# Kernel optimization log

Measured on AMD Instinct MI355X. Metric: run time of the kernel, lower is better.

## Reference

```python
import jax, jax.numpy as jnp
import numpy as np

EPS = 1e-12
N, C, B = 8, 2048, 2048


def setup_inputs() -> dict:
    key = jax.random.key(0)
    kx, kk, kq = jax.random.split(key, 3)
    # Xavier-uniform bound for [C,C] weight
    bound = float(np.sqrt(6.0 / (C + C)))
    X = jax.random.normal(kx, (N, C, B), dtype=jnp.float32)
    Wk = jax.random.uniform(kk, (C, C), minval=-bound, maxval=bound, dtype=jnp.float32)
    Wq = jax.random.uniform(kq, (C, C), minval=-bound, maxval=bound, dtype=jnp.float32)
    Wk0 = jnp.zeros((C, 1), dtype=jnp.float32)
    Wq0 = jnp.zeros((C, 1), dtype=jnp.float32)
    return {"X": X, "Wk": Wk, "Wq": Wq, "Wk0": Wk0, "Wq0": Wq0}


def reference(X, Wk, Wq, Wk0, Wq0):
    # X: [N,C,B]; Wk,Wq: [C,C]; Wk0,Wq0: [C,1] (broadcast over B)
    K = jnp.einsum('ij,njb->nib', Wk, X) + Wk0  # [N,C,B]
    Q = jnp.einsum('ij,njb->nib', Wq, X) + Wq0  # [N,C,B]
    DK2 = jnp.sum(K * K, axis=2)  # [N,C] squared row norms
    DQ2 = jnp.sum(Q * Q, axis=2)  # [N,C]
    DQK = jnp.sqrt(jnp.maximum(DQ2[:, :, None] * DK2[:, None, :], EPS))  # [N,C,C]
    Y = jnp.einsum('nib,njb->nij', Q, K) / DQK  # cosine-normalized scores [N,C,C]
    SM = jax.nn.softmax(Y, axis=1)  # softmax over query-channel axis
    # Z = (X^T @ SM)^T : Z[n,j,b] = sum_c X[n,c,b] * SM[n,c,j]
    Z = jnp.einsum('ncb,ncj->njb', X, SM)  # [N,C,B]
    return Z
```

## Files before the change

kernel.cpp:

```cpp
#include <hip/hip_runtime.h>
#include <hip/hip_bf16.h>

typedef __bf16 bf16_t;
typedef __bf16 bf16x8 __attribute__((ext_vector_type(8)));
typedef __bf16 bf16x4 __attribute__((ext_vector_type(4)));
typedef float  f32x4  __attribute__((ext_vector_type(4)));

#define NB 8
#define CD 2048
#define BD 2048
#define LD 2048
#define BK 64
#define NT (LD / BK)
#define NP (NT / 2)

#define BAR()     __builtin_amdgcn_s_barrier()
#define WAITV(n)  asm volatile("s_waitcnt vmcnt(" #n ")" ::: "memory")
#define M_DSRD 0x100
#define M_MFMA 0x008

template <int NRD>
__device__ __forceinline__ void ilv_pattern() {
#pragma unroll
    for (int g = 0; g < 4; ++g) {
        __builtin_amdgcn_sched_group_barrier(M_DSRD, NRD, 0);
        __builtin_amdgcn_sched_group_barrier(M_MFMA, 4, 0);
    }
}

__global__ void k_transpose_x(const float* __restrict__ X, bf16_t* __restrict__ XbT) {
    __shared__ bf16_t tile[64][66];
    const int t = threadIdx.x;
    const int b0 = blockIdx.x * 64, c0 = blockIdx.y * 64, n = blockIdx.z;
    const float* Xn = X + (size_t)n * CD * BD;
    bf16_t* Tn = XbT + (size_t)n * BD * CD;
    const int cl = t & 63, rw = t >> 6;
#pragma unroll
    for (int r = 0; r < 16; ++r) {
        int row = r * 4 + rw;
        tile[row][cl] = (bf16_t)Xn[(size_t)(c0 + row) * BD + b0 + cl];
    }
    __syncthreads();
#pragma unroll
    for (int r = 0; r < 16; ++r) {
        int row = r * 4 + rw;
        Tn[(size_t)(b0 + row) * CD + c0 + cl] = tile[cl][row];
    }
}

__global__ void k_convert_w(const float* __restrict__ Wk, const float* __restrict__ Wq,
                            bf16_t* __restrict__ Wkb, bf16_t* __restrict__ Wqb) {
    const size_t i = ((size_t)blockIdx.x * 256 + threadIdx.x) * 4;
    const float* src = blockIdx.y ? Wq : Wk;
    bf16_t* dst = blockIdx.y ? Wqb : Wkb;
    float4 v = *(const float4*)(src + i);
    bf16x4 o;
    o[0] = (bf16_t)v.x; o[1] = (bf16_t)v.y; o[2] = (bf16_t)v.z; o[3] = (bf16_t)v.w;
    *(bf16x4*)(dst + i) = o;
}


__device__ __forceinline__ void gll16(const bf16_t* g, bf16_t* l) {
    __builtin_amdgcn_global_load_lds((const __attribute__((address_space(1))) void*)g,
                                     (__attribute__((address_space(3))) void*)l, 16, 0, 0);
}

__device__ __forceinline__ void stage_half(const bf16_t* gsrc, bf16_t* ldsh, int w, int l) {
    const int rr = l >> 3;
    const int ce = ((l & 7) ^ rr) * 8;
#pragma unroll
    for (int i = 0; i < 2; ++i) {
        const bf16_t* g = gsrc + (size_t)(i * 64 + w * 8 + rr) * LD + ce;
        gll16(g, ldsh + i * 4096 + w * 512);
    }
}

__device__ __forceinline__ bf16x8 lds_frag(const bf16_t* hbase, int row16, int lr, int st, int ks, int swz) {
    const int r = row16 + lr;
    const int ce = (st * 32 + ks * 8) ^ swz;
    return *(const bf16x8*)(hbase + r * 64 + ce);
}

template <int EPI>
__global__ __launch_bounds__(512, 2) void k_gemm256(const bf16_t* __restrict__ Aall, size_t sA,
                                                    const bf16_t* __restrict__ Ball, size_t sB,
                                                    void* __restrict__ Call, size_t sC,
                                                    const float* __restrict__ bias) {
    __shared__ alignas(16) bf16_t As[2][2][128 * 64];
    __shared__ alignas(16) bf16_t Bs[2][2][128 * 64];
    const int tid = threadIdx.x;
    const int lane = tid & 63, wave = tid >> 6;
    const int wm = wave >> 2, wn = wave & 3;
    const int lr = lane & 15, ks = lane >> 4;
    const int swz = (lr & 7) << 3;

    const int bid = blockIdx.x;
    const int lin = (bid & 7) * 64 + (bid >> 3);
    const int z = lin >> 6, rem = lin & 63, bm = rem >> 3, bn = rem & 7;
    const int m0 = bm * 256, n0 = bn * 256;

    const bf16_t* Ab = Aall + sA * z + (size_t)m0 * LD;
    const bf16_t* Bb = Ball + sB * z + (size_t)n0 * LD;

    stage_half(Ab,                 &As[0][0][0], wave, lane);
    stage_half(Bb,                 &Bs[0][0][0], wave, lane);
    stage_half(Ab + 128 * LD,      &As[0][1][0], wave, lane);
    stage_half(Bb + 128 * LD,      &Bs[0][1][0], wave, lane);
    WAITV(4);
    stage_half(Ab + BK,            &As[1][0][0], wave, lane);
    stage_half(Bb + BK,            &Bs[1][0][0], wave, lane);
    stage_half(Bb + 128 * LD + BK, &Bs[1][1][0], wave, lane);
    WAITV(6);
    BAR();

    f32x4 acc[2][2][4][2] = {};
    bf16x8 afrE[4][2], afrO[4][2], bf0[2][2], bf1[2][2];

    auto RD_A = [&](bf16x8 (&dst)[4][2], int slot, int half) {
#pragma unroll
        for (int mi = 0; mi < 4; ++mi)
#pragma unroll
            for (int st = 0; st < 2; ++st)
                dst[mi][st] = lds_frag(&As[slot][half][0], wm * 64 + mi * 16, lr, st, ks, swz);
    };
    auto RD_B = [&](bf16x8 (&dst)[2][2], int slot, int half) {
#pragma unroll
        for (int ni = 0; ni < 2; ++ni)
#pragma unroll
            for (int st = 0; st < 2; ++st)
                dst[ni][st] = lds_frag(&Bs[slot][half][0], wn * 32 + ni * 16, lr, st, ks, swz);
    };
    auto MFMA_Q = [&](int mh, int nh, bf16x8 (&asrc)[4][2], bf16x8 (&bsrc)[2][2]) {
#pragma unroll
        for (int st = 0; st < 2; ++st)
#pragma unroll
            for (int mi = 0; mi < 4; ++mi)
#pragma unroll
                for (int ni = 0; ni < 2; ++ni)
                    acc[mh][nh][mi][ni] = __builtin_amdgcn_mfma_f32_16x16x32_bf16(
                        asrc[mi][st], bsrc[ni][st], acc[mh][nh][mi][ni], 0, 0, 0);
    };

    RD_A(afrE, 0, 0); RD_B(bf0, 0, 0);

    for (int tp = 0; tp < NP; ++tp) {
        const int u = 2 * tp, v = u + 1;
        const int w = (u + 2 < NT) ? u + 2 : NT - 1;
        const int x = (v + 2 < NT) ? v + 2 : NT - 1;

        stage_half(Ab + 128 * LD + v * BK, &As[1][1][0], wave, lane);
        BAR();
        __builtin_amdgcn_s_setprio(1);
        RD_B(bf1, 0, 1);
        MFMA_Q(0, 0, afrE, bf0);
        ilv_pattern<1>();
        __builtin_amdgcn_s_setprio(0);
        BAR();

        stage_half(Ab + w * BK, &As[0][0][0], wave, lane);
        BAR();
        __builtin_amdgcn_s_setprio(1);
        RD_A(afrO, 0, 1);
        MFMA_Q(0, 1, afrE, bf1);
        ilv_pattern<2>();
        __builtin_amdgcn_s_setprio(0);
        BAR();

        stage_half(Bb + w * BK, &Bs[0][0][0], wave, lane);
        BAR();
        __builtin_amdgcn_s_setprio(1);
        MFMA_Q(1, 0, afrO, bf0);
        __builtin_amdgcn_s_setprio(0);
        BAR();

        stage_half(Bb + 128 * LD + w * BK, &Bs[0][1][0], wave, lane);
        WAITV(6);
        BAR();
        __builtin_amdgcn_s_setprio(1);
        RD_A(afrE, 1, 0); RD_B(bf0, 1, 0);
        MFMA_Q(1, 1, afrO, bf1);
        ilv_pattern<3>();
        __builtin_amdgcn_s_setprio(0);
        BAR();

        stage_half(Ab + 128 * LD + w * BK, &As[0][1][0], wave, lane);
        BAR();
        __builtin_amdgcn_s_setprio(1);
        RD_B(bf1, 1, 1);
        MFMA_Q(0, 0, afrE, bf0);
        ilv_pattern<1>();
        __builtin_amdgcn_s_setprio(0);
        BAR();

        stage_half(Ab + x * BK, &As[1][0][0], wave, lane);
        BAR();
        __builtin_amdgcn_s_setprio(1);
        RD_A(afrO, 1, 1);
        MFMA_Q(0, 1, afrE, bf1);
        ilv_pattern<2>();
        __builtin_amdgcn_s_setprio(0);
        BAR();

        stage_half(Bb + x * BK, &Bs[1][0][0], wave, lane);
        BAR();
        __builtin_amdgcn_s_setprio(1);
        MFMA_Q(1, 0, afrO, bf0);
        __builtin_amdgcn_s_setprio(0);
        BAR();

        stage_half(Bb + 128 * LD + x * BK, &Bs[1][1][0], wave, lane);
        WAITV(6);
        BAR();
        __builtin_amdgcn_s_setprio(1);
        RD_A(afrE, 0, 0); RD_B(bf0, 0, 0);
        MFMA_Q(1, 1, afrO, bf1);
        ilv_pattern<3>();
        __builtin_amdgcn_s_setprio(0);
        BAR();
    }
    WAITV(0);

    const int rsub = ks * 4;
#pragma unroll
    for (int mh = 0; mh < 2; ++mh)
#pragma unroll
        for (int mi = 0; mi < 4; ++mi)
#pragma unroll
            for (int j = 0; j < 4; ++j) {
                const int r = m0 + mh * 128 + wm * 64 + mi * 16 + rsub + j;
                float bv = 0.f;
                if (EPI == 1) bv = bias[r];
#pragma unroll
                for (int nh = 0; nh < 2; ++nh)
#pragma unroll
                    for (int ni = 0; ni < 2; ++ni) {
                        const int c = n0 + nh * 128 + wn * 32 + ni * 16 + lr;
                        const float vv = acc[mh][nh][mi][ni][j] + bv;
                        if (EPI == 0) ((float*)Call)[sC * z + (size_t)r * LD + c] = vv;
                        else          ((bf16_t*)Call)[sC * z + (size_t)r * LD + c] = (bf16_t)vv;
                    }
            }
}

__global__ void k_row_norm2(const bf16_t* __restrict__ Kb, const bf16_t* __restrict__ Qb,
                            float* __restrict__ DK2, float* __restrict__ DQ2) {
    const int row = blockIdx.x, n = blockIdx.y;
    const bf16_t* src = blockIdx.z ? Qb : Kb;
    float* dst = blockIdx.z ? DQ2 : DK2;
    const bf16_t* pr = src + ((size_t)n * CD + row) * BD + threadIdx.x * 8;
    bf16x8 v = *(const bf16x8*)pr;
    float s = 0.f;
#pragma unroll
    for (int e = 0; e < 8; ++e) { float x = (float)v[e]; s += x * x; }
#pragma unroll
    for (int off = 32; off; off >>= 1) s += __shfl_xor(s, off, 64);
    __shared__ float ws[4];
    if ((threadIdx.x & 63) == 0) ws[threadIdx.x >> 6] = s;
    __syncthreads();
    if (threadIdx.x == 0) dst[(size_t)n * CD + row] = ws[0] + ws[1] + ws[2] + ws[3];
}

__global__ void k_softmax_rows(const bf16_t* __restrict__ Yt, const float* __restrict__ DK2,
                               const float* __restrict__ DQ2, bf16_t* __restrict__ SMT) {
    const int j = blockIdx.x, n = blockIdx.y, t = threadIdx.x;
    const int lane = t & 63, wave = t >> 6;
    const bf16_t* y = Yt + ((size_t)n * CD + j) * CD;
    const float* q2 = DQ2 + (size_t)n * CD;
    const float dk2 = DK2[(size_t)n * CD + j];
    const int i0 = t * 8;

    bf16x8 yr = *(const bf16x8*)(y + i0);
    float4 qa = *(const float4*)(q2 + i0);
    float4 qb = *(const float4*)(q2 + i0 + 4);
    float qv[8] = {qa.x, qa.y, qa.z, qa.w, qb.x, qb.y, qb.z, qb.w};
    float v[8];
#pragma unroll
    for (int e = 0; e < 8; ++e)
        v[e] = (float)yr[e] * rsqrtf(fmaxf(dk2 * qv[e], 1e-12f));

    float m = v[0];
#pragma unroll
    for (int e = 1; e < 8; ++e) m = fmaxf(m, v[e]);
#pragma unroll
    for (int off = 32; off; off >>= 1) m = fmaxf(m, __shfl_xor(m, off, 64));
    __shared__ float redm[4], reds[4];
    if (lane == 0) redm[wave] = m;
    __syncthreads();
    m = fmaxf(fmaxf(redm[0], redm[1]), fmaxf(redm[2], redm[3]));

    float e8[8];
    float s = 0.f;
#pragma unroll
    for (int e = 0; e < 8; ++e) { e8[e] = __expf(v[e] - m); s += e8[e]; }
#pragma unroll
    for (int off = 32; off; off >>= 1) s += __shfl_xor(s, off, 64);
    if (lane == 0) reds[wave] = s;
    __syncthreads();
    s = reds[0] + reds[1] + reds[2] + reds[3];
    const float inv = 1.f / s;

    bf16x8 o;
#pragma unroll
    for (int e = 0; e < 8; ++e) o[e] = (bf16_t)(e8[e] * inv);
    *(bf16x8*)(SMT + ((size_t)n * CD + j) * CD + i0) = o;
}

extern "C" void kernel_launch(void* const* d_in, const int* in_sizes, int n_in,
                              void* d_out, int out_size, void* d_ws, size_t ws_size,
                              hipStream_t stream) {
    const float* X   = (const float*)d_in[0];
    const float* Wk  = (const float*)d_in[1];
    const float* Wq  = (const float*)d_in[2];
    const float* Wk0 = (const float*)d_in[3];
    const float* Wq0 = (const float*)d_in[4];
    float* Z = (float*)d_out;

    const size_t NCB = (size_t)NB * CD * BD;
    const size_t CC  = (size_t)CD * CD;
    const size_t NCC = (size_t)NB * CC;

    char* p = (char*)d_ws;
    bf16_t* XbT = (bf16_t*)p; p += NCB * 2;
    bf16_t* Wkb = (bf16_t*)p; p += CC * 2;
    bf16_t* Wqb = (bf16_t*)p; p += CC * 2;
    bf16_t* Kb  = (bf16_t*)p; p += NCB * 2;
    bf16_t* Qb  = (bf16_t*)p; p += NCB * 2;
    float*  DK2 = (float*)p;  p += (size_t)NB * CD * 4;
    float*  DQ2 = (float*)p;  p += (size_t)NB * CD * 4;
    bf16_t* Yt  = (bf16_t*)p; p += NCC * 2;
    bf16_t* SMT = Kb;
    if ((size_t)(p - (char*)d_ws) > ws_size) return;

    dim3 blk(256);
    k_transpose_x<<<dim3(BD / 64, CD / 64, NB), blk, 0, stream>>>(X, XbT);
    k_convert_w<<<dim3(CC / 1024, 2), blk, 0, stream>>>(Wk, Wq, Wkb, Wqb);
    k_gemm256<1><<<512, 512, 0, stream>>>(Wkb, 0, XbT, (size_t)BD * CD, Kb, (size_t)CD * BD, Wk0);
    k_gemm256<1><<<512, 512, 0, stream>>>(Wqb, 0, XbT, (size_t)BD * CD, Qb, (size_t)CD * BD, Wq0);
    k_row_norm2<<<dim3(CD, NB, 2), blk, 0, stream>>>(Kb, Qb, DK2, DQ2);
    k_gemm256<2><<<512, 512, 0, stream>>>(Kb, (size_t)CD * BD, Qb, (size_t)CD * BD, Yt, CC, nullptr);
    k_softmax_rows<<<dim3(CD, NB), blk, 0, stream>>>(Yt, DK2, DQ2, SMT);
    k_gemm256<0><<<512, 512, 0, stream>>>(SMT, CC, XbT, (size_t)BD * CD, Z, (size_t)CD * BD, nullptr);
}
```

Baseline: 560.2 us.

## Switch GEMMs to 32x32x16 MFMA and fuse K/Q projections into one launch

```diff
diff --git a/kernel.cpp b/kernel.cpp
--- a/kernel.cpp
+++ b/kernel.cpp
@@ -4,7 +4,7 @@
 typedef __bf16 bf16_t;
 typedef __bf16 bf16x8 __attribute__((ext_vector_type(8)));
 typedef __bf16 bf16x4 __attribute__((ext_vector_type(4)));
-typedef float  f32x4  __attribute__((ext_vector_type(4)));
+typedef float  f32x16 __attribute__((ext_vector_type(16)));
 
 #define NB 8
 #define CD 2048
@@ -24,7 +24,7 @@
 #pragma unroll
     for (int g = 0; g < 4; ++g) {
         __builtin_amdgcn_sched_group_barrier(M_DSRD, NRD, 0);
-        __builtin_amdgcn_sched_group_barrier(M_MFMA, 4, 0);
+        __builtin_amdgcn_sched_group_barrier(M_MFMA, 2, 0);
     }
 }
 
@@ -49,14 +49,22 @@
 }
 
 __global__ void k_convert_w(const float* __restrict__ Wk, const float* __restrict__ Wq,
-                            bf16_t* __restrict__ Wkb, bf16_t* __restrict__ Wqb) {
+                            const float* __restrict__ Wk0, const float* __restrict__ Wq0,
+                            bf16_t* __restrict__ Wkqb, float* __restrict__ bias4096) {
     const size_t i = ((size_t)blockIdx.x * 256 + threadIdx.x) * 4;
     const float* src = blockIdx.y ? Wq : Wk;
-    bf16_t* dst = blockIdx.y ? Wqb : Wkb;
+    bf16_t* dst = Wkqb + (blockIdx.y ? (size_t)CD * CD : 0);
     float4 v = *(const float4*)(src + i);
     bf16x4 o;
     o[0] = (bf16_t)v.x; o[1] = (bf16_t)v.y; o[2] = (bf16_t)v.z; o[3] = (bf16_t)v.w;
     *(bf16x4*)(dst + i) = o;
+    if (blockIdx.x == 0) {
+        const float* b0 = blockIdx.y ? Wq0 : Wk0;
+        float* bd = bias4096 + (size_t)blockIdx.y * CD;
+#pragma unroll
+        for (int e = 0; e < 2; ++e)
+            *(float4*)(bd + threadIdx.x * 8 + e * 4) = *(const float4*)(b0 + threadIdx.x * 8 + e * 4);
+    }
 }
 
 
@@ -75,13 +83,7 @@
     }
 }
 
-__device__ __forceinline__ bf16x8 lds_frag(const bf16_t* hbase, int row16, int lr, int st, int ks, int swz) {
-    const int r = row16 + lr;
-    const int ce = (st * 32 + ks * 8) ^ swz;
-    return *(const bf16x8*)(hbase + r * 64 + ce);
-}
-
-template <int EPI>
+template <int EPI, int MBLK>
 __global__ __launch_bounds__(512, 2) void k_gemm256(const bf16_t* __restrict__ Aall, size_t sA,
                                                     const bf16_t* __restrict__ Ball, size_t sB,
                                                     void* __restrict__ Call, size_t sC,
@@ -91,12 +93,14 @@
     const int tid = threadIdx.x;
     const int lane = tid & 63, wave = tid >> 6;
     const int wm = wave >> 2, wn = wave & 3;
-    const int lr = lane & 15, ks = lane >> 4;
-    const int swz = (lr & 7) << 3;
-
+    const int l31 = lane & 31, kg = lane >> 5;
+    const int swz = (lane & 7) << 3;
+
+    constexpr int TPZ = MBLK * 8;
+    constexpr int CPX = NB * TPZ / 8;
     const int bid = blockIdx.x;
-    const int lin = (bid & 7) * 64 + (bid >> 3);
-    const int z = lin >> 6, rem = lin & 63, bm = rem >> 3, bn = rem & 7;
+    const int lin = (bid & 7) * CPX + (bid >> 3);
+    const int z = lin / TPZ, rem = lin % TPZ, bm = rem >> 3, bn = rem & 7;
     const int m0 = bm * 256, n0 = bn * 256;
 
     const bf16_t* Ab = Aall + sA * z + (size_t)m0 * LD;
@@ -113,32 +117,30 @@
     WAITV(6);
     BAR();
 
-    f32x4 acc[2][2][4][2] = {};
-    bf16x8 afrE[4][2], afrO[4][2], bf0[2][2], bf1[2][2];
-
-    auto RD_A = [&](bf16x8 (&dst)[4][2], int slot, int half) {
-#pragma unroll
-        for (int mi = 0; mi < 4; ++mi)
-#pragma unroll
-            for (int st = 0; st < 2; ++st)
-                dst[mi][st] = lds_frag(&As[slot][half][0], wm * 64 + mi * 16, lr, st, ks, swz);
+    f32x16 acc[2][2][2] = {};
+    bf16x8 afrE[2][4], afrO[2][4], bf0[4], bf1[4];
+
+    auto RD_A = [&](bf16x8 (&dst)[2][4], int slot, int half) {
+#pragma unroll
+        for (int mi2 = 0; mi2 < 2; ++mi2)
+#pragma unroll
+            for (int kq = 0; kq < 4; ++kq)
+                dst[mi2][kq] = *(const bf16x8*)(&As[slot][half][0] +
+                    (wm * 64 + mi2 * 32 + l31) * 64 + ((kq * 16 + kg * 8) ^ swz));
     };
-    auto RD_B = [&](bf16x8 (&dst)[2][2], int slot, int half) {
-#pragma unroll
-        for (int ni = 0; ni < 2; ++ni)
-#pragma unroll
-            for (int st = 0; st < 2; ++st)
-                dst[ni][st] = lds_frag(&Bs[slot][half][0], wn * 32 + ni * 16, lr, st, ks, swz);
+    auto RD_B = [&](bf16x8 (&dst)[4], int slot, int half) {
+#pragma unroll
+        for (int kq = 0; kq < 4; ++kq)
+            dst[kq] = *(const bf16x8*)(&Bs[slot][half][0] +
+                (wn * 32 + l31) * 64 + ((kq * 16 + kg * 8) ^ swz));
     };
-    auto MFMA_Q = [&](int mh, int nh, bf16x8 (&asrc)[4][2], bf16x8 (&bsrc)[2][2]) {
-#pragma unroll
-        for (int st = 0; st < 2; ++st)
-#pragma unroll
-            for (int mi = 0; mi < 4; ++mi)
-#pragma unroll
-                for (int ni = 0; ni < 2; ++ni)
-                    acc[mh][nh][mi][ni] = __builtin_amdgcn_mfma_f32_16x16x32_bf16(
-                        asrc[mi][st], bsrc[ni][st], acc[mh][nh][mi][ni], 0, 0, 0);
+    auto MFMA_Q = [&](int mh, int nh, bf16x8 (&asrc)[2][4], bf16x8 (&bsrc)[4]) {
+#pragma unroll
+        for (int kq = 0; kq < 4; ++kq)
+#pragma unroll
+            for (int mi2 = 0; mi2 < 2; ++mi2)
+                acc[mh][nh][mi2] = __builtin_amdgcn_mfma_f32_32x32x16_bf16(
+                    asrc[mi2][kq], bsrc[kq], acc[mh][nh][mi2], 0, 0, 0);
     };
 
     RD_A(afrE, 0, 0); RD_B(bf0, 0, 0);
@@ -220,34 +222,33 @@
     }
     WAITV(0);
 
-    const int rsub = ks * 4;
 #pragma unroll
     for (int mh = 0; mh < 2; ++mh)
 #pragma unroll
-        for (int mi = 0; mi < 4; ++mi)
-#pragma unroll
-            for (int j = 0; j < 4; ++j) {
-                const int r = m0 + mh * 128 + wm * 64 + mi * 16 + rsub + j;
+        for (int mi2 = 0; mi2 < 2; ++mi2) {
+            const int rb = m0 + mh * 128 + wm * 64 + mi2 * 32 + 4 * kg;
+#pragma unroll
+            for (int reg = 0; reg < 16; ++reg) {
+                const int r = rb + (reg & 3) + 8 * (reg >> 2);
                 float bv = 0.f;
                 if (EPI == 1) bv = bias[r];
 #pragma unroll
-                for (int nh = 0; nh < 2; ++nh)
-#pragma unroll
-                    for (int ni = 0; ni < 2; ++ni) {
-                        const int c = n0 + nh * 128 + wn * 32 + ni * 16 + lr;
-                        const float vv = acc[mh][nh][mi][ni][j] + bv;
-                        if (EPI == 0) ((float*)Call)[sC * z + (size_t)r * LD + c] = vv;
-                        else          ((bf16_t*)Call)[sC * z + (size_t)r * LD + c] = (bf16_t)vv;
-                    }
+                for (int nh = 0; nh < 2; ++nh) {
+                    const int c = n0 + nh * 128 + wn * 32 + l31;
+                    const float vv = acc[mh][nh][mi2][reg] + bv;
+                    if (EPI == 0) ((float*)Call)[sC * z + (size_t)r * LD + c] = vv;
+                    else          ((bf16_t*)Call)[sC * z + (size_t)r * LD + c] = (bf16_t)vv;
+                }
             }
-}
-
-__global__ void k_row_norm2(const bf16_t* __restrict__ Kb, const bf16_t* __restrict__ Qb,
+        }
+}
+
+__global__ void k_row_norm2(const bf16_t* __restrict__ KQb,
                             float* __restrict__ DK2, float* __restrict__ DQ2) {
     const int row = blockIdx.x, n = blockIdx.y;
-    const bf16_t* src = blockIdx.z ? Qb : Kb;
     float* dst = blockIdx.z ? DQ2 : DK2;
-    const bf16_t* pr = src + ((size_t)n * CD + row) * BD + threadIdx.x * 8;
+    const bf16_t* pr = KQb + (size_t)n * 2 * CD * BD + (size_t)blockIdx.z * CD * BD
+                     + (size_t)row * BD + threadIdx.x * 8;
     bf16x8 v = *(const bf16x8*)pr;
     float s = 0.f;
 #pragma unroll
@@ -318,26 +319,25 @@
     const size_t NCB = (size_t)NB * CD * BD;
     const size_t CC  = (size_t)CD * CD;
     const size_t NCC = (size_t)NB * CC;
+    const size_t CB  = (size_t)CD * BD;
 
     char* p = (char*)d_ws;
-    bf16_t* XbT = (bf16_t*)p; p += NCB * 2;
-    bf16_t* Wkb = (bf16_t*)p; p += CC * 2;
-    bf16_t* Wqb = (bf16_t*)p; p += CC * 2;
-    bf16_t* Kb  = (bf16_t*)p; p += NCB * 2;
-    bf16_t* Qb  = (bf16_t*)p; p += NCB * 2;
-    float*  DK2 = (float*)p;  p += (size_t)NB * CD * 4;
-    float*  DQ2 = (float*)p;  p += (size_t)NB * CD * 4;
-    bf16_t* Yt  = (bf16_t*)p; p += NCC * 2;
-    bf16_t* SMT = Kb;
+    bf16_t* XbT  = (bf16_t*)p; p += NCB * 2;
+    bf16_t* Wkqb = (bf16_t*)p; p += 2 * CC * 2;
+    bf16_t* KQb  = (bf16_t*)p; p += 2 * NCB * 2;
+    float*  DK2  = (float*)p;  p += (size_t)NB * CD * 4;
+    float*  DQ2  = (float*)p;  p += (size_t)NB * CD * 4;
+    bf16_t* Yt   = (bf16_t*)p; p += NCC * 2;
+    float*  bias4096 = (float*)p; p += 4096 * 4;
+    bf16_t* SMT = (bf16_t*)KQb;
     if ((size_t)(p - (char*)d_ws) > ws_size) return;
 
     dim3 blk(256);
     k_transpose_x<<<dim3(BD / 64, CD / 64, NB), blk, 0, stream>>>(X, XbT);
-    k_convert_w<<<dim3(CC / 1024, 2), blk, 0, stream>>>(Wk, Wq, Wkb, Wqb);
-    k_gemm256<1><<<512, 512, 0, stream>>>(Wkb, 0, XbT, (size_t)BD * CD, Kb, (size_t)CD * BD, Wk0);
-    k_gemm256<1><<<512, 512, 0, stream>>>(Wqb, 0, XbT, (size_t)BD * CD, Qb, (size_t)CD * BD, Wq0);
-    k_row_norm2<<<dim3(CD, NB, 2), blk, 0, stream>>>(Kb, Qb, DK2, DQ2);
-    k_gemm256<2><<<512, 512, 0, stream>>>(Kb, (size_t)CD * BD, Qb, (size_t)CD * BD, Yt, CC, nullptr);
+    k_convert_w<<<dim3(CC / 1024, 2), blk, 0, stream>>>(Wk, Wq, Wk0, Wq0, Wkqb, bias4096);
+    k_gemm256<1, 16><<<NB * 16 * 8, 512, 0, stream>>>(Wkqb, 0, XbT, CB, KQb, 2 * CB, bias4096);
+    k_row_norm2<<<dim3(CD, NB, 2), blk, 0, stream>>>(KQb, DK2, DQ2);
+    k_gemm256<2, 8><<<NB * 8 * 8, 512, 0, stream>>>(KQb, 2 * CB, KQb + CB, 2 * CB, Yt, CC, nullptr);
     k_softmax_rows<<<dim3(CD, NB), blk, 0, stream>>>(Yt, DK2, DQ2, SMT);
-    k_gemm256<0><<<512, 512, 0, stream>>>(SMT, CC, XbT, (size_t)BD * CD, Z, (size_t)CD * BD, nullptr);
-}
+    k_gemm256<0, 8><<<NB * 8 * 8, 512, 0, stream>>>(SMT, CC, XbT, CB, Z, CB, nullptr);
+}
```

Result: slower. 601.7 us (+7.4%).

## Merge K and Q projections into one GEMM and fuse row norms into epilogue

Applied to the files above, without the earlier changes.

```diff
diff --git a/kernel.cpp b/kernel.cpp
--- a/kernel.cpp
+++ b/kernel.cpp
@@ -28,6 +28,10 @@
     }
 }
 
+__global__ void k_zero(float* __restrict__ p) {
+    p[blockIdx.x * 256 + threadIdx.x] = 0.f;
+}
+
 __global__ void k_transpose_x(const float* __restrict__ X, bf16_t* __restrict__ XbT) {
     __shared__ bf16_t tile[64][66];
     const int t = threadIdx.x;
@@ -49,14 +53,22 @@
 }
 
 __global__ void k_convert_w(const float* __restrict__ Wk, const float* __restrict__ Wq,
-                            bf16_t* __restrict__ Wkb, bf16_t* __restrict__ Wqb) {
+                            const float* __restrict__ Wk0, const float* __restrict__ Wq0,
+                            bf16_t* __restrict__ Wkqb, float* __restrict__ bias4096) {
     const size_t i = ((size_t)blockIdx.x * 256 + threadIdx.x) * 4;
     const float* src = blockIdx.y ? Wq : Wk;
-    bf16_t* dst = blockIdx.y ? Wqb : Wkb;
+    bf16_t* dst = Wkqb + (blockIdx.y ? (size_t)CD * CD : 0);
     float4 v = *(const float4*)(src + i);
     bf16x4 o;
     o[0] = (bf16_t)v.x; o[1] = (bf16_t)v.y; o[2] = (bf16_t)v.z; o[3] = (bf16_t)v.w;
     *(bf16x4*)(dst + i) = o;
+    if (blockIdx.x == 0) {
+        const float* b0 = blockIdx.y ? Wq0 : Wk0;
+        float* bd = bias4096 + (size_t)blockIdx.y * CD;
+#pragma unroll
+        for (int e = 0; e < 2; ++e)
+            *(float4*)(bd + threadIdx.x * 8 + e * 4) = *(const float4*)(b0 + threadIdx.x * 8 + e * 4);
+    }
 }
 
 
@@ -81,11 +93,12 @@
     return *(const bf16x8*)(hbase + r * 64 + ce);
 }
 
-template <int EPI>
+template <int EPI, int MBLK>
 __global__ __launch_bounds__(512, 2) void k_gemm256(const bf16_t* __restrict__ Aall, size_t sA,
                                                     const bf16_t* __restrict__ Ball, size_t sB,
                                                     void* __restrict__ Call, size_t sC,
-                                                    const float* __restrict__ bias) {
+                                                    const float* __restrict__ bias,
+                                                    float* __restrict__ norms) {
     __shared__ alignas(16) bf16_t As[2][2][128 * 64];
     __shared__ alignas(16) bf16_t Bs[2][2][128 * 64];
     const int tid = threadIdx.x;
@@ -94,9 +107,11 @@
     const int lr = lane & 15, ks = lane >> 4;
     const int swz = (lr & 7) << 3;
 
+    constexpr int TPZ = MBLK * 8;
+    constexpr int CPX = NB * TPZ / 8;
     const int bid = blockIdx.x;
-    const int lin = (bid & 7) * 64 + (bid >> 3);
-    const int z = lin >> 6, rem = lin & 63, bm = rem >> 3, bn = rem & 7;
+    const int lin = (bid & 7) * CPX + (bid >> 3);
+    const int z = lin / TPZ, rem = lin % TPZ, bm = rem >> 3, bn = rem & 7;
     const int m0 = bm * 256, n0 = bn * 256;
 
     const bf16_t* Ab = Aall + sA * z + (size_t)m0 * LD;
@@ -230,6 +245,7 @@
                 const int r = m0 + mh * 128 + wm * 64 + mi * 16 + rsub + j;
                 float bv = 0.f;
                 if (EPI == 1) bv = bias[r];
+                float sq = 0.f;
 #pragma unroll
                 for (int nh = 0; nh < 2; ++nh)
 #pragma unroll
@@ -238,26 +254,20 @@
                         const float vv = acc[mh][nh][mi][ni][j] + bv;
                         if (EPI == 0) ((float*)Call)[sC * z + (size_t)r * LD + c] = vv;
                         else          ((bf16_t*)Call)[sC * z + (size_t)r * LD + c] = (bf16_t)vv;
+                        if (EPI == 1) sq += vv * vv;
                     }
+                if (EPI == 1) {
+                    sq += __shfl_xor(sq, 1, 64);
+                    sq += __shfl_xor(sq, 2, 64);
+                    sq += __shfl_xor(sq, 4, 64);
+                    sq += __shfl_xor(sq, 8, 64);
+                    if (lr == 0) {
+                        float* nrm = (r < CD) ? norms + (size_t)z * CD + r
+                                              : norms + (size_t)(NB + z) * CD + (r - CD);
+                        atomicAdd(nrm, sq);
+                    }
+                }
             }
-}
-
-__global__ void k_row_norm2(const bf16_t* __restrict__ Kb, const bf16_t* __restrict__ Qb,
-                            float* __restrict__ DK2, float* __restrict__ DQ2) {
-    const int row = blockIdx.x, n = blockIdx.y;
-    const bf16_t* src = blockIdx.z ? Qb : Kb;
-    float* dst = blockIdx.z ? DQ2 : DK2;
-    const bf16_t* pr = src + ((size_t)n * CD + row) * BD + threadIdx.x * 8;
-    bf16x8 v = *(const bf16x8*)pr;
-    float s = 0.f;
-#pragma unroll
-    for (int e = 0; e < 8; ++e) { float x = (float)v[e]; s += x * x; }
-#pragma unroll
-    for (int off = 32; off; off >>= 1) s += __shfl_xor(s, off, 64);
-    __shared__ float ws[4];
-    if ((threadIdx.x & 63) == 0) ws[threadIdx.x >> 6] = s;
-    __syncthreads();
-    if (threadIdx.x == 0) dst[(size_t)n * CD + row] = ws[0] + ws[1] + ws[2] + ws[3];
 }
 
 __global__ void k_softmax_rows(const bf16_t* __restrict__ Yt, const float* __restrict__ DK2,
@@ -318,26 +328,25 @@
     const size_t NCB = (size_t)NB * CD * BD;
     const size_t CC  = (size_t)CD * CD;
     const size_t NCC = (size_t)NB * CC;
+    const size_t CB  = (size_t)CD * BD;
 
     char* p = (char*)d_ws;
-    bf16_t* XbT = (bf16_t*)p; p += NCB * 2;
-    bf16_t* Wkb = (bf16_t*)p; p += CC * 2;
-    bf16_t* Wqb = (bf16_t*)p; p += CC * 2;
-    bf16_t* Kb  = (bf16_t*)p; p += NCB * 2;
-    bf16_t* Qb  = (bf16_t*)p; p += NCB * 2;
-    float*  DK2 = (float*)p;  p += (size_t)NB * CD * 4;
-    float*  DQ2 = (float*)p;  p += (size_t)NB * CD * 4;
-    bf16_t* Yt  = (bf16_t*)p; p += NCC * 2;
-    bf16_t* SMT = Kb;
+    bf16_t* XbT  = (bf16_t*)p; p += NCB * 2;
+    bf16_t* Wkqb = (bf16_t*)p; p += 2 * CC * 2;
+    bf16_t* KQb  = (bf16_t*)p; p += 2 * NCB * 2;
+    float*  DK2  = (float*)p;  p += (size_t)NB * CD * 4;
+    float*  DQ2  = (float*)p;  p += (size_t)NB * CD * 4;
+    bf16_t* Yt   = (bf16_t*)p; p += NCC * 2;
+    float*  bias4096 = (float*)p; p += 4096 * 4;
+    bf16_t* SMT = (bf16_t*)KQb;
     if ((size_t)(p - (char*)d_ws) > ws_size) return;
 
     dim3 blk(256);
+    k_zero<<<2 * NB * CD / 256, blk, 0, stream>>>(DK2);
     k_transpose_x<<<dim3(BD / 64, CD / 64, NB), blk, 0, stream>>>(X, XbT);
-    k_convert_w<<<dim3(CC / 1024, 2), blk, 0, stream>>>(Wk, Wq, Wkb, Wqb);
-    k_gemm256<1><<<512, 512, 0, stream>>>(Wkb, 0, XbT, (size_t)BD * CD, Kb, (size_t)CD * BD, Wk0);
-    k_gemm256<1><<<512, 512, 0, stream>>>(Wqb, 0, XbT, (size_t)BD * CD, Qb, (size_t)CD * BD, Wq0);
-    k_row_norm2<<<dim3(CD, NB, 2), blk, 0, stream>>>(Kb, Qb, DK2, DQ2);
-    k_gemm256<2><<<512, 512, 0, stream>>>(Kb, (size_t)CD * BD, Qb, (size_t)CD * BD, Yt, CC, nullptr);
+    k_convert_w<<<dim3(CC / 1024, 2), blk, 0, stream>>>(Wk, Wq, Wk0, Wq0, Wkqb, bias4096);
+    k_gemm256<1, 16><<<NB * 16 * 8, 512, 0, stream>>>(Wkqb, 0, XbT, CB, KQb, 2 * CB, bias4096, DK2);
+    k_gemm256<2, 8><<<NB * 8 * 8, 512, 0, stream>>>(KQb, 2 * CB, KQb + CB, 2 * CB, Yt, CC, nullptr, nullptr);
     k_softmax_rows<<<dim3(CD, NB), blk, 0, stream>>>(Yt, DK2, DQ2, SMT);
-    k_gemm256<0><<<512, 512, 0, stream>>>(SMT, CC, XbT, (size_t)BD * CD, Z, (size_t)CD * BD, nullptr);
-}
+    k_gemm256<0, 8><<<NB * 8 * 8, 512, 0, stream>>>(SMT, CC, XbT, CB, Z, CB, nullptr, nullptr);
+}
```

Result: slower. 578.1 us (+3.2%).
